# Performance work log

Measured on AMD Instinct MI355X. Metric: run time of the kernel, lower is better.

## Reference

```python
import jax, jax.numpy as jnp
import numpy as np

N, D, S, M = 16, 64, 32, 48  # batch, in_dim, out_dim, set size
BASIS = 4

def setup_inputs() -> dict:
    key = jax.random.key(0)
    k1, k2 = jax.random.split(key, 2)
    x = jax.random.normal(k1, (N, D, M), dtype=jnp.float32)
    scale = np.sqrt(2.0 / (D + S + BASIS)).astype(np.float32)
    coefs = scale * jax.random.normal(k2, (D, S, BASIS), dtype=jnp.float32)
    bias = jnp.zeros((1, S, 1, 1, 1), dtype=jnp.float32)
    return {"x": x, "coefs": coefs, "bias": bias}

def reference(x, coefs, bias):
    # Fused form of: ops = eset_ops_1_to_3(x) -> (N,D,4,m,m,m); out = einsum('dsb,ndbijk->nsijk', coefs, ops) + bias
    # Basis patterns (broadcast/diagonal):
    #   b=0: ops[n,d,0,i,j,k] = x[n,d,i]   (broadcast over j,k)
    #   b=1: ops[n,d,1,i,j,k] = x[n,d,j]   (broadcast over i,k)
    #   b=2: ops[n,d,2,i,j,k] = x[n,d,k]   (broadcast over i,j)
    #   b=3: ops[n,d,3,i,i,i] = x[n,d,i]   (superdiagonal), 0 elsewhere
    # Contract coefs with x first -> tiny (4, N, S, m) tensor, then broadcast.
    m = x.shape[-1]
    t = jnp.einsum('dsb,ndm->bnsm', coefs, x)  # (4, N, S, m)
    t0, t1, t2, t3 = t
    out = (t0[:, :, :, None, None]    # broadcast over j,k
           + t1[:, :, None, :, None]  # broadcast over i,k
           + t2[:, :, None, None, :]) # broadcast over i,j
    r = jnp.arange(m)
    out = out.at[:, :, r, r, r].add(t3)  # superdiagonal placement
    return out + bias
```

## Files before the change

kernel.cpp:

```cpp
#include <hip/hip_runtime.h>

#define NN 16
#define DD 64
#define SS 32
#define MM 48

typedef float floatx4 __attribute__((ext_vector_type(4)));

__global__ __launch_bounds__(576, 1) void eq1to3_kernel(
    const float* __restrict__ x,
    const float* __restrict__ coefs,
    const float* __restrict__ bias,
    float* __restrict__ out)
{
    __shared__ float t_lds[4][MM];

    const int ns = blockIdx.x;
    const int n  = ns / SS;
    const int s  = ns % SS;
    const int tid = threadIdx.x;

    if (tid < 4 * MM) {
        const int m = tid % MM;
        const int b = tid / MM;
        const float* xp = x + (size_t)n * DD * MM + m;
        const float* cp = coefs + s * 4 + b;
        float acc = 0.f;
        #pragma unroll 8
        for (int d = 0; d < DD; ++d) {
            acc += cp[(size_t)d * SS * 4] * xp[(size_t)d * MM];
        }
        t_lds[b][m] = acc;
    }
    __syncthreads();

    const int j  = tid / (MM / 4);
    const int k4 = tid % (MM / 4);

    const float bs  = bias[s];
    const float t1j = t_lds[1][j];
    floatx4 base;
    base.x = t_lds[2][4 * k4 + 0] + t1j + bs;
    base.y = t_lds[2][4 * k4 + 1] + t1j + bs;
    base.z = t_lds[2][4 * k4 + 2] + t1j + bs;
    base.w = t_lds[2][4 * k4 + 3] + t1j + bs;

    floatx4 dvec = {0.f, 0.f, 0.f, 0.f};
    if ((j >> 2) == k4) dvec[j & 3] = t_lds[3][j];

    floatx4* outp = (floatx4*)(out + (size_t)ns * MM * MM * MM + j * MM + 4 * k4);
    const int plane4 = MM * MM / 4;

    #pragma unroll 4
    for (int i = 0; i < MM; ++i) {
        const float t0i = t_lds[0][i];
        floatx4 v = base + t0i;
        if (i == j) v += dvec;
        outp[(size_t)i * plane4] = v;
    }
}

extern "C" void kernel_launch(void* const* d_in, const int* in_sizes, int n_in,
                              void* d_out, int out_size, void* d_ws, size_t ws_size,
                              hipStream_t stream) {
    const float* x     = (const float*)d_in[0];
    const float* coefs = (const float*)d_in[1];
    const float* bias  = (const float*)d_in[2];
    float* out = (float*)d_out;

    eq1to3_kernel<<<dim3(NN * SS), dim3(576), 0, stream>>>(x, coefs, bias, out);
}
```

Before: 224.8 us.

## Split into contraction kernel and fully parallel coalesced broadcast-store kernel

Moves the small coefs-x contraction into its own kernel that writes the four basis tables (with bias folded into one) to workspace. A second kernel, launched over many small blocks, has each thread produce float4 outputs for four batch-slot pairs by reading the cached tables. This replaces the old 512 large blocks, each streaming hundreds of KB serially, and aims to raise memory-level parallelism. In exchange it adds a second launch and workspace traffic for the tables.

```diff
diff --git a/kernel.cpp b/kernel.cpp
--- a/kernel.cpp
+++ b/kernel.cpp
@@ -4,59 +4,62 @@
 #define DD 64
 #define SS 32
 #define MM 48
+#define NSB (NN*SS)
+#define TBL (NSB*MM)
 
 typedef float floatx4 __attribute__((ext_vector_type(4)));
 
-__global__ __launch_bounds__(576, 1) void eq1to3_kernel(
+__global__ __launch_bounds__(192, 1) void eq1to3_tk(
     const float* __restrict__ x,
     const float* __restrict__ coefs,
     const float* __restrict__ bias,
-    float* __restrict__ out)
+    float* __restrict__ t)
 {
-    __shared__ float t_lds[4][MM];
-
     const int ns = blockIdx.x;
     const int n  = ns / SS;
     const int s  = ns % SS;
-    const int tid = threadIdx.x;
+    const int b  = threadIdx.x / MM;
+    const int m  = threadIdx.x % MM;
 
-    if (tid < 4 * MM) {
-        const int m = tid % MM;
-        const int b = tid / MM;
-        const float* xp = x + (size_t)n * DD * MM + m;
-        const float* cp = coefs + s * 4 + b;
-        float acc = 0.f;
-        #pragma unroll 8
-        for (int d = 0; d < DD; ++d) {
-            acc += cp[(size_t)d * SS * 4] * xp[(size_t)d * MM];
-        }
-        t_lds[b][m] = acc;
-    }
-    __syncthreads();
+    const float* xp = x + (size_t)n * DD * MM + m;
+    const float* cp = coefs + s * 4 + b;
+    float acc = 0.f;
+    #pragma unroll 8
+    for (int d = 0; d < DD; ++d)
+        acc += cp[(size_t)d * SS * 4] * xp[(size_t)d * MM];
 
-    const int j  = tid / (MM / 4);
-    const int k4 = tid % (MM / 4);
+    if (b == 1) acc += bias[s];
+    t[b * TBL + ns * MM + m] = acc;
+}
 
-    const float bs  = bias[s];
-    const float t1j = t_lds[1][j];
-    floatx4 base;
-    base.x = t_lds[2][4 * k4 + 0] + t1j + bs;
-    base.y = t_lds[2][4 * k4 + 1] + t1j + bs;
-    base.z = t_lds[2][4 * k4 + 2] + t1j + bs;
-    base.w = t_lds[2][4 * k4 + 3] + t1j + bs;
+__global__ __launch_bounds__(256, 1) void eq1to3_store(
+    const float* __restrict__ t,
+    float* __restrict__ out)
+{
+    const unsigned g = blockIdx.x * 256u + threadIdx.x;
+    const unsigned k4  = g % 12u;
+    const unsigned r1  = g / 12u;
+    const unsigned j   = r1 % (unsigned)MM;
+    const unsigned r2  = r1 / (unsigned)MM;
+    const unsigned i   = r2 % (unsigned)MM;
+    const unsigned ns0 = r2 / (unsigned)MM;
 
-    floatx4 dvec = {0.f, 0.f, 0.f, 0.f};
-    if ((j >> 2) == k4) dvec[j & 3] = t_lds[3][j];
+    const float*   t0  = t;
+    const float*   t1  = t + TBL;
+    const floatx4* t2q = (const floatx4*)(t + 2 * TBL);
+    const float*   t3  = t + 3 * TBL;
 
-    floatx4* outp = (floatx4*)(out + (size_t)ns * MM * MM * MM + j * MM + 4 * k4);
-    const int plane4 = MM * MM / 4;
+    const bool diag = (i == j) && ((j >> 2) == k4);
+    const int  dl   = j & 3;
+    floatx4* out4 = (floatx4*)out;
 
-    #pragma unroll 4
-    for (int i = 0; i < MM; ++i) {
-        const float t0i = t_lds[0][i];
-        floatx4 v = base + t0i;
-        if (i == j) v += dvec;
-        outp[(size_t)i * plane4] = v;
+    #pragma unroll
+    for (int p = 0; p < 4; ++p) {
+        const unsigned ns = ns0 + 128u * p;
+        floatx4 v = t2q[ns * 12u + k4];
+        v += t0[ns * MM + i] + t1[ns * MM + j];
+        if (diag) v[dl] += t3[ns * MM + j];
+        out4[(size_t)ns * (MM*MM*MM/4) + i * (MM*MM/4) + j * (MM/4) + k4] = v;
     }
 }
 
@@ -67,6 +70,8 @@
     const float* coefs = (const float*)d_in[1];
     const float* bias  = (const float*)d_in[2];
     float* out = (float*)d_out;
+    float* t   = (float*)d_ws;
 
-    eq1to3_kernel<<<dim3(NN * SS), dim3(576), 0, stream>>>(x, coefs, bias, out);
+    eq1to3_tk<<<dim3(NSB), dim3(192), 0, stream>>>(x, coefs, bias, t);
+    eq1to3_store<<<dim3(NN*SS*MM*MM*MM/4/4/256), dim3(256), 0, stream>>>(t, out);
 }
```

Measured after the change: 222.0 us. About the same (-1.2%).
